# Optimization experiments

Hardware: AMD Instinct MI355X
Metric: run time of the kernel (lower is better)

Reference implementation:

```python
import jax, jax.numpy as jnp
import numpy as np

D_MODEL = 1024
H = 16
D_K = D_MODEL // H  # 64
B, S = 2, 2048


def setup_inputs() -> dict:
    key = jax.random.key(0)
    ks = jax.random.split(key, 8)
    scale = 1.0 / np.sqrt(D_MODEL)
    return {
        "q": jax.random.normal(ks[0], (B, S, D_MODEL), dtype=jnp.float32),
        "k": jax.random.normal(ks[1], (B, S, D_MODEL), dtype=jnp.float32),
        "v": jax.random.normal(ks[2], (B, S, D_MODEL), dtype=jnp.float32),
        "W_q": jax.random.normal(ks[3], (H, D_MODEL, D_K), dtype=jnp.float32) * scale,
        "W_k": jax.random.normal(ks[4], (H, D_MODEL, D_K), dtype=jnp.float32) * scale,
        "W_v": jax.random.normal(ks[5], (H, D_MODEL, D_K), dtype=jnp.float32) * scale,
        "W_o": jax.random.normal(ks[6], (D_MODEL, H * D_K), dtype=jnp.float32) * scale,
        "b_o": jnp.zeros((D_MODEL,), dtype=jnp.float32),
    }


def reference(q, k, v, W_q, W_k, W_v, W_o, b_o):
    b, s, _ = q.shape
    h, _, d_k = W_q.shape
    inv_sqrt_dk = jnp.asarray(1.0 / np.sqrt(d_k), q.dtype)
    # per-head projections: [b, h, s, d_k]
    qh = jnp.einsum("bsd,hdk->bhsk", q, W_q)
    kh = jnp.einsum("bsd,hdk->bhsk", k, W_k)
    vh = jnp.einsum("bsd,hdk->bhsk", v, W_v)
    # scaled dot product attention
    scores = jnp.einsum("bhqk,bhsk->bhqs", qh, kh) * inv_sqrt_dk  # [b,h,S,S]
    attn = jax.nn.softmax(scores, axis=-1)
    ctx = jnp.einsum("bhqs,bhsk->bhqk", attn, vh)  # [b,h,S,d_k]
    # chunk over heads + concat along feature dim -> [b, S, h*d_k], head-major
    ctx = ctx.transpose(0, 2, 1, 3).reshape(b, s, h * d_k)
    # final linear
    return ctx @ W_o.T + b_o
```

## Files before the change

### kernel.cpp

```cpp
#include <hip/hip_runtime.h>
#include <cstdint>
#include <cstddef>


typedef unsigned short bf16_t;
typedef __attribute__((ext_vector_type(8))) short short8;
typedef __attribute__((ext_vector_type(4))) float f32x4;

__device__ __forceinline__ uint32_t fbits(float f) {
  union { float f; uint32_t u; } v; v.f = f; return v.u;
}
__device__ __forceinline__ bf16_t f2bf(float f) {
  uint32_t u = fbits(f);
  return (bf16_t)((u + 0x7FFFu + ((u >> 16) & 1u)) >> 16);
}
__device__ __forceinline__ uint32_t packbf2(float lo, float hi) {
  uint32_t a = fbits(hi) + 0x8000u;
  uint32_t b = fbits(lo) + 0x8000u;
  return __builtin_amdgcn_perm(a, b, 0x07060302u);
}
__device__ __forceinline__ int4 cvt8(f32x4 lo, f32x4 hi) {
  return make_int4((int)packbf2(lo.x, lo.y), (int)packbf2(lo.z, lo.w),
                   (int)packbf2(hi.x, hi.y), (int)packbf2(hi.z, hi.w));
}

__device__ __forceinline__ void gload16(const bf16_t* g, bf16_t* l) {
  __builtin_amdgcn_global_load_lds(
      (const __attribute__((address_space(1))) void*)g,
      (__attribute__((address_space(3))) void*)l, 16, 0, 0);
}

__global__ void prep_kernel(const float* __restrict__ Wo,
                            const float* __restrict__ Wq, const float* __restrict__ Wk,
                            const float* __restrict__ Wv,
                            const float* __restrict__ q, const float* __restrict__ k,
                            const float* __restrict__ v,
                            bf16_t* __restrict__ Woo,
                            bf16_t* __restrict__ Wtq, bf16_t* __restrict__ Wtk,
                            bf16_t* __restrict__ Wtv,
                            bf16_t* __restrict__ qb, bf16_t* __restrict__ kb,
                            bf16_t* __restrict__ vb) {
  int blk = blockIdx.x;
  int tid = threadIdx.x;
  if (blk < 1024) {
    int i = blk * 256 + tid;
    f32x4 val = ((const f32x4*)Wo)[i];
    ushort4 o;
    o.x = f2bf(val.x); o.y = f2bf(val.y); o.z = f2bf(val.z); o.w = f2bf(val.w);
    ((ushort4*)Woo)[i] = o;
  } else if (blk < 2560) {
    int blk2 = blk - 1024;
    int z = blk2 >> 9, t = blk2 & 511;
    const float* W = z == 0 ? Wq : z == 1 ? Wk : Wv;
    bf16_t* Wt = z == 0 ? Wtq : z == 1 ? Wtk : Wtv;
    int h = t >> 5, d0 = (t & 31) * 32;
    __shared__ float tile[32][65];
    const float* src = W + ((size_t)h << 16) + (size_t)d0 * 64;
    int d = tid >> 3;
#pragma unroll
    for (int j = 0; j < 2; j++) {
      int dk = (tid & 7) * 8 + j * 4;
      *(f32x4*)&tile[d][dk] = *(const f32x4*)(src + d * 64 + dk);
    }
    __syncthreads();
    int dk2 = tid >> 2, c = tid & 3;
    union { ushort s[8]; int4 v; } o;
#pragma unroll
    for (int j = 0; j < 8; j++) o.s[j] = f2bf(tile[c * 8 + j][dk2]);
    *(int4*)(Wt + (size_t)(h * 64 + dk2) * 1024 + d0 + c * 8) = o.v;
  } else {
    int blk3 = blk - 2560;
    int z = blk3 >> 11;
    int t3 = blk3 & 2047;
    const float* src = z == 0 ? q : z == 1 ? k : v;
    bf16_t* dst = z == 0 ? qb : z == 1 ? kb : vb;
    int i = t3 * 256 + tid;
    f32x4 lo = ((const f32x4*)src)[i * 2];
    f32x4 hi = ((const f32x4*)src)[i * 2 + 1];
    ((int4*)dst)[i] = cvt8(lo, hi);
  }
}

__global__ __launch_bounds__(256) void gemm_proj_kernel(
    const bf16_t* __restrict__ A0, const bf16_t* __restrict__ A1, const bf16_t* __restrict__ A2,
    const bf16_t* __restrict__ B0, const bf16_t* __restrict__ B1, const bf16_t* __restrict__ B2,
    bf16_t* __restrict__ O0, bf16_t* __restrict__ O1, bf16_t* __restrict__ O2,
    float s0)
{
  const int bid = blockIdx.x;
  const int nIdx = bid / 96;
  const int g = bid - nIdx * 96;
  const int z = g % 3;
  const int m0 = (g / 3) * 128, n0 = nIdx * 128;

  const bf16_t* A  = z == 0 ? A0 : z == 1 ? A1 : A2;
  const bf16_t* Bt = z == 0 ? B0 : z == 1 ? B1 : B2;
  bf16_t* Cout     = z == 0 ? O0 : z == 1 ? O1 : O2;
  const float scale = z == 0 ? s0 : 1.0f;
  const int K = 1024;

  __shared__ alignas(16) bf16_t smem[18432];

  const int tid = threadIdx.x;
  const int lane = tid & 63, wave = tid >> 6;
  const int wm = wave >> 1, wn = wave & 1;
  const int quad = lane >> 4, l15 = lane & 15;

  f32x4 acc[4][4];
#pragma unroll
  for (int i = 0; i < 4; i++)
#pragma unroll
    for (int j = 0; j < 4; j++) acc[i][j] = (f32x4)0.0f;

  const int srow = tid >> 2, scol = (tid & 3) * 8;
  const bf16_t* pa0 = A  + (size_t)(m0 + srow) * K + scol;
  const bf16_t* pa1 = pa0 + (size_t)64 * K;
  const bf16_t* pb0 = Bt + (size_t)(n0 + srow) * K + scol;
  const bf16_t* pb1 = pb0 + (size_t)64 * K;
  const int lws = wave * 512;

  gload16(pa0, smem + lws);
  gload16(pa1, smem + 2048 + lws);
  gload16(pb0, smem + 4096 + lws);
  gload16(pb1, smem + 6144 + lws);
  __syncthreads();

  for (int it = 0; it < 32; ++it) {
    const int cur = (it & 1) * 8192;
    if (it < 31) {
      const int nxt = ((it + 1) & 1) * 8192;
      const int ko = (it + 1) * 32;
      gload16(pa0 + ko, smem + nxt + lws);
      gload16(pa1 + ko, smem + nxt + 2048 + lws);
      gload16(pb0 + ko, smem + nxt + 4096 + lws);
      gload16(pb1 + ko, smem + nxt + 6144 + lws);
    }

    short8 af[4], bfr[4];
#pragma unroll
    for (int mi = 0; mi < 4; mi++)
      af[mi] = *(const short8*)(smem + cur + (wm * 64 + mi * 16 + l15) * 32 + quad * 8);
#pragma unroll
    for (int ni = 0; ni < 4; ni++)
      bfr[ni] = *(const short8*)(smem + cur + 4096 + (wn * 64 + ni * 16 + l15) * 32 + quad * 8);
#pragma unroll
    for (int mi = 0; mi < 4; mi++)
#pragma unroll
      for (int ni = 0; ni < 4; ni++)
        acc[mi][ni] = __builtin_amdgcn_mfma_f32_16x16x32_bf16(af[mi], bfr[ni], acc[mi][ni], 0, 0, 0);

    __syncthreads();
  }

  const int s0r = m0 & 2047, bb = m0 >> 11, hp = n0 >> 6;
  if (z < 2) {
    bf16_t* slot = smem + wn * 9216;
#pragma unroll
    for (int ni = 0; ni < 4; ni++)
#pragma unroll
      for (int mi = 0; mi < 4; mi++)
#pragma unroll
        for (int r = 0; r < 4; r++)
          slot[(wm * 64 + mi * 16 + quad * 4 + r) * 72 + ni * 16 + l15] =
              f2bf(acc[mi][ni][r] * scale);
    __syncthreads();
#pragma unroll
    for (int rd = 0; rd < 8; ++rd) {
      int idx = rd * 256 + tid;
      int si = idx >> 10, mm = (idx >> 3) & 127, c8 = idx & 7;
      int4 val = *(const int4*)(smem + si * 9216 + mm * 72 + c8 * 8);
      *(int4*)(Cout + ((size_t)((bb * 16 + hp + si) * 2048 + s0r + mm)) * 64 + c8 * 8) = val;
    }
  } else {
    bf16_t* slot = smem + wn * 8704;
#pragma unroll
    for (int ni = 0; ni < 4; ni++)
#pragma unroll
      for (int mi = 0; mi < 4; mi++) {
        uint2 pk = make_uint2(packbf2(acc[mi][ni][0], acc[mi][ni][1]),
                              packbf2(acc[mi][ni][2], acc[mi][ni][3]));
        *(uint2*)(slot + (ni * 16 + l15) * 136 + wm * 64 + mi * 16 + quad * 4) = pk;
      }
    __syncthreads();
#pragma unroll
    for (int rd = 0; rd < 8; ++rd) {
      int idx = rd * 256 + tid;
      int si = idx >> 10, c = (idx >> 4) & 63, ck = idx & 15;
      int4 val = *(const int4*)(smem + si * 8704 + c * 136 + ck * 8);
      *(int4*)(Cout + (size_t)(bb * 16 + hp + si) * 131072 + (size_t)c * 2048 + s0r + ck * 8) = val;
    }
  }
}

__global__ __launch_bounds__(256) void gemm_out_kernel(
    const bf16_t* __restrict__ A, const bf16_t* __restrict__ Bt,
    float* __restrict__ C, const float* __restrict__ bias)
{
  const int K = 1024, N = 1024;
  __shared__ alignas(16) bf16_t smem[12288];
  const int tid = threadIdx.x;
  const int lane = tid & 63, wave = tid >> 6;
  const int quad = lane >> 4, l15 = lane & 15;
  const int m0 = (blockIdx.x & 31) * 128, n0 = (blockIdx.x >> 5) * 64;

  f32x4 acc[2][4];
#pragma unroll
  for (int i = 0; i < 2; i++)
#pragma unroll
    for (int j = 0; j < 4; j++) acc[i][j] = (f32x4)0.0f;

  const int srow = tid >> 2, scol = (tid & 3) * 8;
  const bf16_t* pa0 = A  + (size_t)(m0 + srow) * K + scol;
  const bf16_t* pa1 = pa0 + (size_t)64 * K;
  const bf16_t* pb  = Bt + (size_t)(n0 + srow) * K + scol;
  const int lws = wave * 512;

  gload16(pa0, smem + lws);
  gload16(pa1, smem + 2048 + lws);
  gload16(pb,  smem + 4096 + lws);
  __syncthreads();

  for (int it = 0; it < 32; ++it) {
    const int cur = (it & 1) * 6144;
    if (it < 31) {
      const int nxt = ((it + 1) & 1) * 6144;
      const int ko = (it + 1) * 32;
      gload16(pa0 + ko, smem + nxt + lws);
      gload16(pa1 + ko, smem + nxt + 2048 + lws);
      gload16(pb + ko,  smem + nxt + 4096 + lws);
    }

    short8 af[2], bfr[4];
#pragma unroll
    for (int mi = 0; mi < 2; mi++)
      af[mi] = *(const short8*)(smem + cur + (wave * 32 + mi * 16 + l15) * 32 + quad * 8);
#pragma unroll
    for (int ni = 0; ni < 4; ni++)
      bfr[ni] = *(const short8*)(smem + cur + 4096 + (ni * 16 + l15) * 32 + quad * 8);
#pragma unroll
    for (int mi = 0; mi < 2; mi++)
#pragma unroll
      for (int ni = 0; ni < 4; ni++)
        acc[mi][ni] = __builtin_amdgcn_mfma_f32_16x16x32_bf16(af[mi], bfr[ni], acc[mi][ni], 0, 0, 0);

    __syncthreads();
  }

#pragma unroll
  for (int ni = 0; ni < 4; ni++) {
    int col = n0 + ni * 16 + l15;
    float bv = bias[col];
#pragma unroll
    for (int mi = 0; mi < 2; mi++) {
      int row = m0 + wave * 32 + mi * 16 + quad * 4;
#pragma unroll
      for (int r = 0; r < 4; r++)
        C[(size_t)(row + r) * N + col] = acc[mi][ni][r] + bv;
    }
  }
}

__global__ __launch_bounds__(512) void flash_kernel(
    const bf16_t* __restrict__ qh, const bf16_t* __restrict__ kh,
    const bf16_t* __restrict__ vT, bf16_t* __restrict__ ctx)
{
  __shared__ alignas(16) bf16_t KtF[2][4096];
  __shared__ alignas(16) bf16_t VtF[2][4096];
  __shared__ alignas(16) bf16_t PtF[8192];
  const int tid = threadIdx.x, lane = tid & 63, wave = tid >> 6;
  const int quad = lane >> 4, l15 = lane & 15;
  const int gid = blockIdx.x;
  const int hb = gid & 31;
  const int h = hb & 15, b = hb >> 4;
  const int q0 = (gid >> 5) * 128;
  const size_t headoff = (size_t)hb * 2048 * 64;
  const bf16_t* Q = qh + headoff;
  const bf16_t* K = kh + headoff;
  const bf16_t* V = vT + headoff;

  short8 qf[2];
#pragma unroll
  for (int ks = 0; ks < 2; ks++)
    qf[ks] = *(const short8*)(Q + (size_t)(q0 + wave * 16 + l15) * 64
                              + ks * 32 + quad * 8);

  f32x4 O[4];
#pragma unroll
  for (int mi = 0; mi < 4; mi++) O[mi] = (f32x4)0.0f;
  f32x4 lacc = (f32x4)0.0f;

  const bf16_t* Kp = K + (size_t)((wave >> 1) * 16 + l15) * 64 + (wave & 1) * 32 + quad * 8;
  const bf16_t* Vp = V + (size_t)((wave >> 1) * 16 + l15) * 2048 + (wave & 1) * 32 + quad * 8;
  const int soff = wave * 512 + lane * 8;
  const int pwb = wave * 2048 + ((quad >> 1) * 16 + l15) * 16 + 8 * (quad & 1);

  auto body = [&](int buf) {
    f32x4 S[4];
#pragma unroll
    for (int mi = 0; mi < 4; mi++) S[mi] = (f32x4)0.0f;
#pragma unroll
    for (int ks = 0; ks < 2; ks++) {
#pragma unroll
      for (int mi = 0; mi < 4; mi++) {
        short8 kf = *(const short8*)(&KtF[buf][(mi * 2 + ks) * 512 + lane * 8]);
        S[mi] = __builtin_amdgcn_mfma_f32_16x16x32_bf16(kf, qf[ks], S[mi], 0, 0, 0);
      }
    }
#pragma unroll
    for (int mi = 0; mi < 4; mi++)
#pragma unroll
      for (int r = 0; r < 4; r++)
        S[mi][r] = __builtin_amdgcn_exp2f(S[mi][r]);
    lacc += (S[0] + S[1]) + (S[2] + S[3]);
#pragma unroll
    for (int mi = 0; mi < 4; mi++) {
      uint2 pk = make_uint2(packbf2(S[mi][0], S[mi][1]),
                            packbf2(S[mi][2], S[mi][3]));
      *(uint2*)((char*)PtF + pwb + (mi >> 1) * 1024 + (mi & 1) * 512) = pk;
    }
#pragma unroll
    for (int ks = 0; ks < 2; ks++) {
      short8 pf = *(const short8*)(&PtF[wave * 1024 + (ks * 64 + lane) * 8]);
#pragma unroll
      for (int mi = 0; mi < 4; mi++) {
        short8 vf = *(const short8*)(&VtF[buf][(mi * 2 + ks) * 512 + lane * 8]);
        O[mi] = __builtin_amdgcn_mfma_f32_16x16x32_bf16(vf, pf, O[mi], 0, 0, 0);
      }
    }
  };

  int4 k0 = *(const int4*)Kp, v0 = *(const int4*)Vp;
  *(int4*)(&KtF[0][soff]) = k0;
  *(int4*)(&VtF[0][soff]) = v0;
  int4 kA = *(const int4*)(Kp + 4096), vA = *(const int4*)(Vp + 64);
  __syncthreads();

  for (int it = 0; it < 32; it += 2) {
    *(int4*)(&KtF[1][soff]) = kA;
    *(int4*)(&VtF[1][soff]) = vA;
    int4 kB, vB;
    if (it + 2 < 32) {
      kB = *(const int4*)(Kp + (size_t)(it + 2) * 4096);
      vB = *(const int4*)(Vp + (size_t)(it + 2) * 64);
    }
    body(0);
    __syncthreads();

    if (it + 2 < 32) {
      *(int4*)(&KtF[0][soff]) = kB;
      *(int4*)(&VtF[0][soff]) = vB;
    }
    if (it + 3 < 32) {
      kA = *(const int4*)(Kp + (size_t)(it + 3) * 4096);
      vA = *(const int4*)(Vp + (size_t)(it + 3) * 64);
    }
    body(1);
    __syncthreads();
  }

  {
    float l = (lacc[0] + lacc[1]) + (lacc[2] + lacc[3]);
    l += __shfl_xor(l, 16, 64);
    l += __shfl_xor(l, 32, 64);
    float inv = 1.0f / l;
    int qrow = q0 + wave * 16 + l15;
    bf16_t* crow = ctx + ((size_t)(b * 2048 + qrow)) * 1024 + h * 64;
#pragma unroll
    for (int mi = 0; mi < 4; mi++) {
      uint2 pk = make_uint2(packbf2(O[mi][0] * inv, O[mi][1] * inv),
                            packbf2(O[mi][2] * inv, O[mi][3] * inv));
      *(uint2*)(crow + mi * 16 + quad * 4) = pk;
    }
  }
}

extern "C" void kernel_launch(void* const* d_in, const int* in_sizes, int n_in,
                              void* d_out, int out_size, void* d_ws, size_t ws_size,
                              hipStream_t stream)
{
  const float* q  = (const float*)d_in[0];
  const float* k  = (const float*)d_in[1];
  const float* v  = (const float*)d_in[2];
  const float* Wq = (const float*)d_in[3];
  const float* Wk = (const float*)d_in[4];
  const float* Wv = (const float*)d_in[5];
  const float* Wo = (const float*)d_in[6];
  const float* bo = (const float*)d_in[7];
  float* out = (float*)d_out;

  const size_t NX = (size_t)4096 * 1024;
  const size_t NW = (size_t)1024 * 1024;

  char* p = (char*)d_ws;
  bf16_t* Wtq = (bf16_t*)p; p += NW * 2;
  bf16_t* Wtk = (bf16_t*)p; p += NW * 2;
  bf16_t* Wtv = (bf16_t*)p; p += NW * 2;
  bf16_t* Wob = (bf16_t*)p; p += NW * 2;
  bf16_t* qb  = (bf16_t*)p; p += NX * 2;
  bf16_t* kb  = (bf16_t*)p; p += NX * 2;
  bf16_t* vb  = (bf16_t*)p; p += NX * 2;
  bf16_t* qhb = (bf16_t*)p; p += NX * 2;
  bf16_t* khb = (bf16_t*)p; p += NX * 2;
  bf16_t* vTb = (bf16_t*)p; p += NX * 2;
  bf16_t* ctxb = (bf16_t*)p; p += NX * 2;

  prep_kernel<<<8704, 256, 0, stream>>>(Wo, Wq, Wk, Wv, q, k, v,
                                        Wob, Wtq, Wtk, Wtv, qb, kb, vb);

  const float qscale = 0.125f * 1.44269504088896340736f;
  gemm_proj_kernel<<<768, 256, 0, stream>>>(qb, kb, vb, Wtq, Wtk, Wtv,
                                            qhb, khb, vTb, qscale);

  flash_kernel<<<512, 512, 0, stream>>>(qhb, khb, vTb, ctxb);

  gemm_out_kernel<<<512, 256, 0, stream>>>(ctxb, Wob, out, bo);

  (void)in_sizes; (void)n_in; (void)out_size; (void)ws_size;
}
```

Baseline: 208.9 us.

## Switch flash attention to 32x32x16 MFMA with register-resident P via permlane32 swap

Rewrites the attention kernel to use 32x32x16 bf16 MFMAs with 4 waves each owning 32 query rows, and changes the K/V projection epilogues to write pre-swizzled fragment-ordered tiles so the flash kernel can copy K/V tiles linearly into LDS. P is repacked into the B operand in registers using permlane32_swap instead of round-tripping through shared memory. The output is staged through swizzled LDS for coalesced stores. This removes the P LDS write/read and uses larger MFMA tiles, at the cost of more registers per thread and half the threads per block.

```diff
diff --git a/kernel.cpp b/kernel.cpp
--- a/kernel.cpp
+++ b/kernel.cpp
@@ -6,6 +6,8 @@
 typedef unsigned short bf16_t;
 typedef __attribute__((ext_vector_type(8))) short short8;
 typedef __attribute__((ext_vector_type(4))) float f32x4;
+typedef __attribute__((ext_vector_type(16))) float f32x16;
+typedef __attribute__((ext_vector_type(2))) unsigned int uint2v;
 
 __device__ __forceinline__ uint32_t fbits(float f) {
   union { float f; uint32_t u; } v; v.f = f; return v.u;
@@ -169,7 +171,16 @@
       int idx = rd * 256 + tid;
       int si = idx >> 10, mm = (idx >> 3) & 127, c8 = idx & 7;
       int4 val = *(const int4*)(smem + si * 9216 + mm * 72 + c8 * 8);
-      *(int4*)(Cout + ((size_t)((bb * 16 + hp + si) * 2048 + s0r + mm)) * 64 + c8 * 8) = val;
+      size_t head = (size_t)(bb * 16 + hp + si);
+      if (z == 0) {
+        *(int4*)(Cout + (head * 2048 + s0r + mm) * 64 + c8 * 8) = val;
+      } else {
+        int row = s0r + mm;
+        int tile = row >> 6, loc = row & 63;
+        int f = (loc >> 5) * 4 + (c8 >> 1);
+        int j = (c8 & 1) * 32 + (loc & 31);
+        *(int4*)(Cout + head * 131072 + (size_t)tile * 4096 + f * 512 + j * 8) = val;
+      }
     }
   } else {
     bf16_t* slot = smem + wn * 8704;
@@ -187,7 +198,11 @@
       int idx = rd * 256 + tid;
       int si = idx >> 10, c = (idx >> 4) & 63, ck = idx & 15;
       int4 val = *(const int4*)(smem + si * 8704 + c * 136 + ck * 8);
-      *(int4*)(Cout + (size_t)(bb * 16 + hp + si) * 131072 + (size_t)c * 2048 + s0r + ck * 8) = val;
+      int kk = s0r + ck * 8;
+      int tile = kk >> 6;
+      int f = (c >> 5) * 4 + ((kk >> 4) & 3);
+      int j = ((kk >> 3) & 1) * 32 + (c & 31);
+      *(int4*)(Cout + (size_t)(bb * 16 + hp + si) * 131072 + (size_t)tile * 4096 + f * 512 + j * 8) = val;
     }
   }
 }
@@ -260,117 +275,140 @@
   }
 }
 
-__global__ __launch_bounds__(512) void flash_kernel(
+__global__ __launch_bounds__(256) void flash_kernel(
     const bf16_t* __restrict__ qh, const bf16_t* __restrict__ kh,
-    const bf16_t* __restrict__ vT, bf16_t* __restrict__ ctx)
+    const bf16_t* __restrict__ vh, bf16_t* __restrict__ ctx)
 {
-  __shared__ alignas(16) bf16_t KtF[2][4096];
-  __shared__ alignas(16) bf16_t VtF[2][4096];
-  __shared__ alignas(16) bf16_t PtF[8192];
+  __shared__ alignas(16) bf16_t smem[16384];
   const int tid = threadIdx.x, lane = tid & 63, wave = tid >> 6;
-  const int quad = lane >> 4, l15 = lane & 15;
+  const int hlf = lane >> 5, l31 = lane & 31;
   const int gid = blockIdx.x;
   const int hb = gid & 31;
   const int h = hb & 15, b = hb >> 4;
   const int q0 = (gid >> 5) * 128;
-  const size_t headoff = (size_t)hb * 2048 * 64;
-  const bf16_t* Q = qh + headoff;
-  const bf16_t* K = kh + headoff;
-  const bf16_t* V = vT + headoff;
-
-  short8 qf[2];
-#pragma unroll
-  for (int ks = 0; ks < 2; ks++)
-    qf[ks] = *(const short8*)(Q + (size_t)(q0 + wave * 16 + l15) * 64
-                              + ks * 32 + quad * 8);
-
-  f32x4 O[4];
-#pragma unroll
-  for (int mi = 0; mi < 4; mi++) O[mi] = (f32x4)0.0f;
-  f32x4 lacc = (f32x4)0.0f;
-
-  const bf16_t* Kp = K + (size_t)((wave >> 1) * 16 + l15) * 64 + (wave & 1) * 32 + quad * 8;
-  const bf16_t* Vp = V + (size_t)((wave >> 1) * 16 + l15) * 2048 + (wave & 1) * 32 + quad * 8;
-  const int soff = wave * 512 + lane * 8;
-  const int pwb = wave * 2048 + ((quad >> 1) * 16 + l15) * 16 + 8 * (quad & 1);
+  const size_t headoff = (size_t)hb * 131072;
+  const bf16_t* Q  = qh + headoff;
+  const bf16_t* Kf = kh + headoff;
+  const bf16_t* Vf = vh + headoff;
+
+  short8 qf[4];
+#pragma unroll
+  for (int dk = 0; dk < 4; dk++)
+    qf[dk] = *(const short8*)(Q + (size_t)(q0 + wave * 32 + l31) * 64 + dk * 16 + hlf * 8);
+
+  f32x16 Oa = (f32x16)0.0f, Ob = (f32x16)0.0f;
+  float lsum = 0.0f;
+
+  const bf16_t* Kp0 = Kf + tid * 8;
+  const bf16_t* Kp1 = Kf + tid * 8 + 2048;
+  const bf16_t* Vp0 = Vf + 4096 - 4096 + tid * 8;
+  const bf16_t* Vp1 = Vf + tid * 8 + 2048;
+  bf16_t* sK = smem + tid * 8;
+  bf16_t* sV = smem + 4096 + tid * 8;
 
   auto body = [&](int buf) {
-    f32x4 S[4];
-#pragma unroll
-    for (int mi = 0; mi < 4; mi++) S[mi] = (f32x4)0.0f;
-#pragma unroll
-    for (int ks = 0; ks < 2; ks++) {
-#pragma unroll
-      for (int mi = 0; mi < 4; mi++) {
-        short8 kf = *(const short8*)(&KtF[buf][(mi * 2 + ks) * 512 + lane * 8]);
-        S[mi] = __builtin_amdgcn_mfma_f32_16x16x32_bf16(kf, qf[ks], S[mi], 0, 0, 0);
+    const bf16_t* Kb = smem + buf * 8192;
+    const bf16_t* Vb = smem + buf * 8192 + 4096;
+    f32x16 S0 = (f32x16)0.0f, S1 = (f32x16)0.0f;
+#pragma unroll
+    for (int dk = 0; dk < 4; dk++) {
+      short8 kf0 = *(const short8*)(Kb + dk * 512 + lane * 8);
+      short8 kf1 = *(const short8*)(Kb + (4 + dk) * 512 + lane * 8);
+      S0 = __builtin_amdgcn_mfma_f32_32x32x16_bf16(kf0, qf[dk], S0, 0, 0, 0);
+      S1 = __builtin_amdgcn_mfma_f32_32x32x16_bf16(kf1, qf[dk], S1, 0, 0, 0);
+    }
+#pragma unroll
+    for (int r = 0; r < 16; r++) {
+      S0[r] = __builtin_amdgcn_exp2f(S0[r]);
+      S1[r] = __builtin_amdgcn_exp2f(S1[r]);
+    }
+    {
+      f32x16 ss = S0 + S1;
+      float a0 = (ss[0] + ss[1]) + (ss[2] + ss[3]);
+      float a1 = (ss[4] + ss[5]) + (ss[6] + ss[7]);
+      float a2 = (ss[8] + ss[9]) + (ss[10] + ss[11]);
+      float a3 = (ss[12] + ss[13]) + (ss[14] + ss[15]);
+      lsum += (a0 + a1) + (a2 + a3);
+    }
+#pragma unroll
+    for (int mi = 0; mi < 2; mi++) {
+      f32x16 P = mi ? S1 : S0;
+#pragma unroll
+      for (int ksl = 0; ksl < 2; ksl++) {
+        const int ks = mi * 2 + ksl, base = ksl * 8;
+        uint32_t X = packbf2(P[base + 0], P[base + 1]);
+        uint32_t Y = packbf2(P[base + 2], P[base + 3]);
+        uint32_t Z = packbf2(P[base + 4], P[base + 5]);
+        uint32_t W = packbf2(P[base + 6], P[base + 7]);
+        uint2v r1 = __builtin_amdgcn_permlane32_swap(X, Z, false, false);
+        uint2v r2 = __builtin_amdgcn_permlane32_swap(Y, W, false, false);
+        int4 bi = make_int4((int)r1.x, (int)r2.x, (int)r1.y, (int)r2.y);
+        short8 Bf = *(short8*)&bi;
+        short8 vf0 = *(const short8*)(Vb + ks * 512 + lane * 8);
+        short8 vf1 = *(const short8*)(Vb + (4 + ks) * 512 + lane * 8);
+        Oa = __builtin_amdgcn_mfma_f32_32x32x16_bf16(vf0, Bf, Oa, 0, 0, 0);
+        Ob = __builtin_amdgcn_mfma_f32_32x32x16_bf16(vf1, Bf, Ob, 0, 0, 0);
       }
     }
-#pragma unroll
-    for (int mi = 0; mi < 4; mi++)
-#pragma unroll
-      for (int r = 0; r < 4; r++)
-        S[mi][r] = __builtin_amdgcn_exp2f(S[mi][r]);
-    lacc += (S[0] + S[1]) + (S[2] + S[3]);
-#pragma unroll
-    for (int mi = 0; mi < 4; mi++) {
-      uint2 pk = make_uint2(packbf2(S[mi][0], S[mi][1]),
-                            packbf2(S[mi][2], S[mi][3]));
-      *(uint2*)((char*)PtF + pwb + (mi >> 1) * 1024 + (mi & 1) * 512) = pk;
-    }
-#pragma unroll
-    for (int ks = 0; ks < 2; ks++) {
-      short8 pf = *(const short8*)(&PtF[wave * 1024 + (ks * 64 + lane) * 8]);
-#pragma unroll
-      for (int mi = 0; mi < 4; mi++) {
-        short8 vf = *(const short8*)(&VtF[buf][(mi * 2 + ks) * 512 + lane * 8]);
-        O[mi] = __builtin_amdgcn_mfma_f32_16x16x32_bf16(vf, pf, O[mi], 0, 0, 0);
-      }
-    }
   };
 
-  int4 k0 = *(const int4*)Kp, v0 = *(const int4*)Vp;
-  *(int4*)(&KtF[0][soff]) = k0;
-  *(int4*)(&VtF[0][soff]) = v0;
-  int4 kA = *(const int4*)(Kp + 4096), vA = *(const int4*)(Vp + 64);
+  int4 k0a = *(const int4*)Kp0, k0b = *(const int4*)Kp1;
+  int4 v0a = *(const int4*)Vp0, v0b = *(const int4*)Vp1;
+  *(int4*)sK = k0a; *(int4*)(sK + 2048) = k0b;
+  *(int4*)sV = v0a; *(int4*)(sV + 2048) = v0b;
+  int4 kAa = *(const int4*)(Kp0 + 4096), kAb = *(const int4*)(Kp1 + 4096);
+  int4 vAa = *(const int4*)(Vp0 + 4096), vAb = *(const int4*)(Vp1 + 4096);
   __syncthreads();
 
   for (int it = 0; it < 32; it += 2) {
-    *(int4*)(&KtF[1][soff]) = kA;
-    *(int4*)(&VtF[1][soff]) = vA;
-    int4 kB, vB;
+    *(int4*)(sK + 8192) = kAa; *(int4*)(sK + 8192 + 2048) = kAb;
+    *(int4*)(sV + 8192) = vAa; *(int4*)(sV + 8192 + 2048) = vAb;
+    int4 kBa, kBb, vBa, vBb;
     if (it + 2 < 32) {
-      kB = *(const int4*)(Kp + (size_t)(it + 2) * 4096);
-      vB = *(const int4*)(Vp + (size_t)(it + 2) * 64);
+      kBa = *(const int4*)(Kp0 + (size_t)(it + 2) * 4096);
+      kBb = *(const int4*)(Kp1 + (size_t)(it + 2) * 4096);
+      vBa = *(const int4*)(Vp0 + (size_t)(it + 2) * 4096);
+      vBb = *(const int4*)(Vp1 + (size_t)(it + 2) * 4096);
     }
     body(0);
     __syncthreads();
 
     if (it + 2 < 32) {
-      *(int4*)(&KtF[0][soff]) = kB;
-      *(int4*)(&VtF[0][soff]) = vB;
+      *(int4*)sK = kBa; *(int4*)(sK + 2048) = kBb;
+      *(int4*)sV = vBa; *(int4*)(sV + 2048) = vBb;
     }
     if (it + 3 < 32) {
-      kA = *(const int4*)(Kp + (size_t)(it + 3) * 4096);
-      vA = *(const int4*)(Vp + (size_t)(it + 3) * 64);
+      kAa = *(const int4*)(Kp0 + (size_t)(it + 3) * 4096);
+      kAb = *(const int4*)(Kp1 + (size_t)(it + 3) * 4096);
+      vAa = *(const int4*)(Vp0 + (size_t)(it + 3) * 4096);
+      vAb = *(const int4*)(Vp1 + (size_t)(it + 3) * 4096);
     }
     body(1);
     __syncthreads();
   }
 
-  {
-    float l = (lacc[0] + lacc[1]) + (lacc[2] + lacc[3]);
-    l += __shfl_xor(l, 16, 64);
-    l += __shfl_xor(l, 32, 64);
-    float inv = 1.0f / l;
-    int qrow = q0 + wave * 16 + l15;
-    bf16_t* crow = ctx + ((size_t)(b * 2048 + qrow)) * 1024 + h * 64;
-#pragma unroll
-    for (int mi = 0; mi < 4; mi++) {
-      uint2 pk = make_uint2(packbf2(O[mi][0] * inv, O[mi][1] * inv),
-                            packbf2(O[mi][2] * inv, O[mi][3] * inv));
-      *(uint2*)(crow + mi * 16 + quad * 4) = pk;
-    }
+  lsum += __shfl_xor(lsum, 32, 64);
+  float inv = 1.0f / lsum;
+  bf16_t* slot = smem + wave * 2048;
+  const int swz = l31 & 7;
+#pragma unroll
+  for (int dmi = 0; dmi < 2; dmi++) {
+    f32x16 Ov = dmi ? Ob : Oa;
+#pragma unroll
+    for (int rq = 0; rq < 4; rq++) {
+      uint2 pk = make_uint2(packbf2(Ov[rq * 4 + 0] * inv, Ov[rq * 4 + 1] * inv),
+                            packbf2(Ov[rq * 4 + 2] * inv, Ov[rq * 4 + 3] * inv));
+      int c = dmi * 4 + rq;
+      *(uint2*)(slot + l31 * 64 + ((c ^ swz) * 8 + 4 * hlf)) = pk;
+    }
+  }
+  __syncthreads();
+#pragma unroll
+  for (int p = 0; p < 4; p++) {
+    int s2 = p * 64 + lane;
+    int qr = s2 >> 3, cr = s2 & 7;
+    int4 val = *(const int4*)(slot + qr * 64 + ((cr ^ (qr & 7)) * 8));
+    *(int4*)(ctx + (size_t)(b * 2048 + q0 + wave * 32 + qr) * 1024 + h * 64 + cr * 8) = val;
   }
 }
 
@@ -411,7 +449,7 @@
   gemm_proj_kernel<<<768, 256, 0, stream>>>(qb, kb, vb, Wtq, Wtk, Wtv,
                                             qhb, khb, vTb, qscale);
 
-  flash_kernel<<<512, 512, 0, stream>>>(qhb, khb, vTb, ctxb);
+  flash_kernel<<<512, 256, 0, stream>>>(qhb, khb, vTb, ctxb);
 
   gemm_out_kernel<<<512, 256, 0, stream>>>(ctxb, Wob, out, bo);
 
```

After: 212.3 us. About the same (+1.6%).
